# Optimization experiments

Measured on AMD Instinct MI355X. Metric: run time of the kernel, lower is better.

The kernel has to match this reference:

```python
import jax, jax.numpy as jnp
import numpy as np

B, H, S, D = 4, 16, 2048, 64
SCALE = 8.0  # sqrt(D)
NEG = -1000000000.0


def setup_inputs() -> dict:
    key = jax.random.key(0)
    kq, kk, kv = jax.random.split(key, 3)
    q = jax.random.normal(kq, (B, H, S, D), dtype=jnp.float32)
    k = jax.random.normal(kk, (B, H, S, D), dtype=jnp.float32)
    v = jax.random.normal(kv, (B, H, S, D), dtype=jnp.float32)
    # causal mask: True means masked out (matches torch masked_fill)
    mask = jnp.triu(jnp.ones((S, S), dtype=bool), k=1)[None, None, :, :]
    mask = jnp.broadcast_to(mask, (B, 1, S, S))
    return {"q": q, "k": k, "v": v, "mask": mask}


def reference(q, k, v, mask):
    # score = q @ k^T / scale  -> [B,H,S,S]
    score = jnp.einsum("bhqd,bhkd->bhqk", q, k) / SCALE
    score = jnp.where(mask, NEG, score)
    probs = jax.nn.softmax(score, axis=-1)
    context = jnp.einsum("bhqk,bhkd->bhqd", probs, v)
    return context
```

## Files before the change

### kernel.cpp

```cpp
#include <hip/hip_runtime.h>

#define SQ 2048
#define DH 64
#define BK 64
#define NQT 32
#define NBH 64
#define M0 8.0f

#define WS_BYTES ((size_t)2 * NBH * SQ * DH * 2)

typedef float f32x4 __attribute__((ext_vector_type(4)));
typedef __bf16 bf16x8 __attribute__((ext_vector_type(8)));
typedef _Float16 f16x4 __attribute__((ext_vector_type(4)));
typedef _Float16 f16x8 __attribute__((ext_vector_type(8)));
typedef __fp16 fp16x2 __attribute__((ext_vector_type(2)));
typedef unsigned short u16x8 __attribute__((ext_vector_type(8)));
typedef unsigned int u32x4 __attribute__((ext_vector_type(4)));

static __device__ __forceinline__ unsigned int pkbf(float a, float b) {
#if __has_builtin(__builtin_amdgcn_cvt_pk_bf16_f32)
  typedef __bf16 bf16x2 __attribute__((ext_vector_type(2)));
  bf16x2 r = __builtin_amdgcn_cvt_pk_bf16_f32(a, b);
  return __builtin_bit_cast(unsigned int, r);
#else
  unsigned int ua = __builtin_bit_cast(unsigned int, a);
  unsigned int ub = __builtin_bit_cast(unsigned int, b);
  ua += 0x7fffu + ((ua >> 16) & 1u);
  ub += 0x7fffu + ((ub >> 16) & 1u);
  return (ua >> 16) | (ub & 0xffff0000u);
#endif
}

static __device__ __forceinline__ unsigned int pkf16(float a, float b) {
  fp16x2 r = __builtin_amdgcn_cvt_pkrtz(a, b);
  return __builtin_bit_cast(unsigned int, r);
}

static __device__ __forceinline__ f32x4 mfma_qk(u16x8 a, u16x8 b, f32x4 c) {
  return __builtin_amdgcn_mfma_f32_16x16x32_bf16(
      __builtin_bit_cast(bf16x8, a), __builtin_bit_cast(bf16x8, b), c, 0, 0, 0);
}

static __device__ __forceinline__ f32x4 mfma_pv(f16x4 a, f16x4 b, f32x4 c) {
  return __builtin_amdgcn_mfma_f32_16x16x16f16(a, b, c, 0, 0, 0);
}

static __device__ __forceinline__ f32x4 mfma_pv32(f16x8 a, f16x8 b, f32x4 c) {
  return __builtin_amdgcn_mfma_f32_16x16x32_f16(a, b, c, 0, 0, 0);
}

static __device__ __forceinline__ void ld16(unsigned short* l, const unsigned short* g) {
  __builtin_amdgcn_global_load_lds(
      (const __attribute__((address_space(1))) unsigned int*)(const void*)g,
      (__attribute__((address_space(3))) unsigned int*)(void*)l, 16, 0, 0);
}

static __device__ __forceinline__ void store_tile(float* wb, float* dst,
                                                  const f32x4* o, int lane,
                                                  int l15, int quad) {
#pragma unroll
  for (int dt = 0; dt < 4; ++dt) {
    const int colw = dt * 16 + quad * 4;
    *(f32x4*)&wb[l15 * 64 + (colw ^ ((l15 & 3) * 16))] = o[dt];
  }
  __builtin_amdgcn_wave_barrier();
#pragma unroll
  for (int j = 0; j < 4; ++j) {
    const int row = j * 4 + (lane >> 4);
    const int colw = (lane & 15) * 4;
    f32x4 v = *(const f32x4*)&wb[row * 64 + (colw ^ ((row & 3) * 16))];
    *(f32x4*)&dst[row * 64 + colw] = v;
  }
}

__global__ __launch_bounds__(256) void prep(const float* __restrict__ K,
                                            const float* __restrict__ V,
                                            unsigned short* __restrict__ Kf,
                                            unsigned short* __restrict__ Vf) {
  const int bh = (int)blockIdx.x >> 5;
  const int st = (int)blockIdx.x & 31;
  const int tid = threadIdx.x;
  __shared__ __align__(16) unsigned short T[DH * 64];
  {
    const int kvb = (tid >> 4) * 4, vdb = (tid & 15) * 4;
    const float* vp = V + ((size_t)bh * SQ + st * 64 + kvb) * DH + vdb;
    f32x4 r0 = *(const f32x4*)vp, r1 = *(const f32x4*)(vp + DH),
          r2 = *(const f32x4*)(vp + 2 * DH), r3 = *(const f32x4*)(vp + 3 * DH);
    const int uu = kvb >> 3, h = (kvb >> 2) & 1;
#pragma unroll
    for (int i = 0; i < 4; ++i) {
      const int d = vdb + i;
      uint2 w = {pkf16(r0[i], r1[i]), pkf16(r2[i], r3[i])};
      *(uint2*)&T[d * 64 + ((uu ^ (d & 7)) * 8) + h * 4] = w;
    }
  }
  {
    const size_t kin = ((size_t)bh * SQ + st * 64) * DH;
    unsigned short* kfo = Kf + (size_t)bh * SQ * DH + (size_t)st * 64 * DH;
#pragma unroll
    for (int e = 0; e < 2; ++e) {
      const int L = tid * 2 + e;
      const int l15 = L & 15, quad = (L >> 4) & 3, c = (L >> 6) & 1, nt = (L >> 7) & 3;
      const int krow = (nt >> 1) * 32 + ((l15 >> 2) & 3) * 8 + (nt & 1) * 4 + (l15 & 3);
      const float* kp = K + kin + (size_t)krow * DH + (c * 4 + quad) * 8;
      f32x4 x = *(const f32x4*)kp, y = *(const f32x4*)(kp + 4);
      u32x4 w = {pkbf(x[0], x[1]), pkbf(x[2], x[3]), pkbf(y[0], y[1]), pkbf(y[2], y[3])};
      *(u32x4*)&kfo[L * 8] = w;
    }
  }
  __syncthreads();
  {
    unsigned short* vfo = Vf + (size_t)bh * SQ * DH + (size_t)st * 64 * DH;
#pragma unroll
    for (int e = 0; e < 2; ++e) {
      const int L = tid * 2 + e;
      const int l15 = L & 15, quad = (L >> 4) & 3, dt = (L >> 6) & 3, n2 = (L >> 8) & 1;
      const int d = dt * 16 + l15, uu = n2 * 4 + quad;
      u16x8 val = *(const u16x8*)&T[d * 64 + ((uu ^ (d & 7)) * 8)];
      *(u16x8*)&vfo[L * 8] = val;
    }
  }
}

__global__ __launch_bounds__(256, 4) void fa_main(
    const float* __restrict__ Q, const unsigned short* __restrict__ Kf,
    const unsigned short* __restrict__ Vf, float* __restrict__ O) {
  const int lin = (int)blockIdx.x;
  const int xcd = lin & 7, u = lin >> 3;
  const int hh = u & 7;
  const int pi = (int)((0x32104567BA98CDEFull >> ((u >> 3) * 4)) & 15u);
  const int bh = hh * 8 + xcd;
  const int tend = 2 * pi + 1;

  const int tid = threadIdx.x;
  const int wv = tid >> 6;
  const int lane = tid & 63;
  const int l15 = lane & 15;
  const int quad = lane >> 4;

  __shared__ __align__(16) unsigned short S0[2 * BK * DH];
  __shared__ __align__(16) unsigned short S1[2 * BK * DH];

  const size_t hq = (size_t)bh * (SQ * DH);
  const unsigned short* KfH = Kf + (size_t)bh * SQ * DH;
  const unsigned short* VfH = Vf + (size_t)bh * SQ * DH;

  const int qbase = pi * 128 + wv * 32;
  const int dtw = 2 * pi + (wv >> 1);
  const int qo = (wv & 1) * 32;

  u16x8 qf[2][2];
  {
    const float scq = 0.125f * 1.4426950408889634f;
#pragma unroll
    for (int f = 0; f < 2; ++f) {
      const float* qp = Q + hq + (size_t)(qbase + 16 * f + l15) * DH + quad * 8;
#pragma unroll
      for (int c = 0; c < 2; ++c) {
        f32x4 x = *(const f32x4*)(qp + c * 32);
        f32x4 y = *(const f32x4*)(qp + c * 32 + 4);
        u32x4 w = {pkbf(x[0] * scq, x[1] * scq), pkbf(x[2] * scq, x[3] * scq),
                   pkbf(y[0] * scq, y[1] * scq), pkbf(y[2] * scq, y[3] * scq)};
        qf[f][c] = __builtin_bit_cast(u16x8, w);
      }
    }
  }

  f32x4 o0[4], o1[4], la0, la1;
#pragma unroll
  for (int dt = 0; dt < 4; ++dt) {
    o0[dt] = (f32x4){0.f, 0.f, 0.f, 0.f};
    o1[dt] = (f32x4){0.f, 0.f, 0.f, 0.f};
  }
  la0 = (f32x4){0.f, 0.f, 0.f, 0.f};
  la1 = (f32x4){0.f, 0.f, 0.f, 0.f};
  const f16x8 ones8 = {(_Float16)1.f, (_Float16)1.f, (_Float16)1.f, (_Float16)1.f,
                       (_Float16)1.f, (_Float16)1.f, (_Float16)1.f, (_Float16)1.f};

  auto stage = [&](unsigned short* W, int t) {
#pragma unroll
    for (int j = 0; j < 2; ++j)
      ld16(&W[j * 2048 + tid * 8], &KfH[(size_t)t * 4096 + j * 2048 + tid * 8]);
#pragma unroll
    for (int j = 0; j < 2; ++j)
      ld16(&W[4096 + j * 2048 + tid * 8],
           &VfH[(size_t)t * 4096 + j * 2048 + tid * 8]);
  };

  auto attend = [&](const unsigned short* B, bool diag) {
    const unsigned short* Ks = B;
    const unsigned short* Vs = B + 4096;
    f32x4 s0[4], s1[4];
    __builtin_amdgcn_s_setprio(1);
#pragma unroll
    for (int nt = 0; nt < 4; ++nt) {
      f32x4 a0 = {-M0, -M0, -M0, -M0}, a1 = {-M0, -M0, -M0, -M0};
#pragma unroll
      for (int c = 0; c < 2; ++c) {
        u16x8 kf = *(const u16x8*)&Ks[(nt * 2 + c) * 512 + lane * 8];
        a0 = mfma_qk(kf, qf[0][c], a0);
        a1 = mfma_qk(kf, qf[1][c], a1);
      }
      s0[nt] = a0;
      s1[nt] = a1;
    }
    __builtin_amdgcn_s_setprio(0);
    if (diag) {
#pragma unroll
      for (int nt = 0; nt < 4; ++nt)
#pragma unroll
        for (int r = 0; r < 4; ++r) {
          const int kvl = (nt >> 1) * 32 + quad * 8 + (nt & 1) * 4 + r;
          if (kvl > qo + l15) s0[nt][r] = -1e30f;
          if (kvl > qo + 16 + l15) s1[nt][r] = -1e30f;
        }
    }
    f16x8 pf0[2], pf1[2];
#pragma unroll
    for (int n2 = 0; n2 < 2; ++n2) {
      f32x4 pe0, po0, pe1, po1;
#pragma unroll
      for (int r = 0; r < 4; ++r) {
        pe0[r] = __builtin_amdgcn_exp2f(s0[2 * n2][r]);
        po0[r] = __builtin_amdgcn_exp2f(s0[2 * n2 + 1][r]);
        pe1[r] = __builtin_amdgcn_exp2f(s1[2 * n2][r]);
        po1[r] = __builtin_amdgcn_exp2f(s1[2 * n2 + 1][r]);
      }
      u32x4 w0 = {pkf16(pe0[0], pe0[1]), pkf16(pe0[2], pe0[3]),
                  pkf16(po0[0], po0[1]), pkf16(po0[2], po0[3])};
      u32x4 w1 = {pkf16(pe1[0], pe1[1]), pkf16(pe1[2], pe1[3]),
                  pkf16(po1[0], po1[1]), pkf16(po1[2], po1[3])};
      pf0[n2] = __builtin_bit_cast(f16x8, w0);
      pf1[n2] = __builtin_bit_cast(f16x8, w1);
    }
    __builtin_amdgcn_s_setprio(1);
#pragma unroll
    for (int n2 = 0; n2 < 2; ++n2) {
      la0 = mfma_pv32(ones8, pf0[n2], la0);
      la1 = mfma_pv32(ones8, pf1[n2], la1);
    }
#pragma unroll
    for (int dt = 0; dt < 4; ++dt) {
#pragma unroll
      for (int n2 = 0; n2 < 2; ++n2) {
        f16x8 vf = *(const f16x8*)&Vs[(n2 * 4 + dt) * 512 + lane * 8];
        o0[dt] = mfma_pv32(vf, pf0[n2], o0[dt]);
        o1[dt] = mfma_pv32(vf, pf1[n2], o1[dt]);
      }
    }
    __builtin_amdgcn_s_setprio(0);
  };

  auto step = [&](int t, const unsigned short* R, unsigned short* W) {
    if (t <= dtw) attend(R, t == dtw);
    __syncthreads();
    if (t + 2 <= tend) stage(W, t + 2);
  };

  stage(S0, 0);
  __syncthreads();
  stage(S1, 1);
  for (int t = 0; t <= tend; t += 2) {
    step(t, S0, S0);
    if (t + 1 <= tend) step(t + 1, S1, S1);
  }

  {
    const float inv0 = 1.0f / la0[0];
    const float inv1 = 1.0f / la1[0];
#pragma unroll
    for (int f = 0; f < 2; ++f) {
      const f32x4* oo = f ? o1 : o0;
      const float inv = f ? inv1 : inv0;
      float* dst = O + hq + (size_t)(qbase + f * 16 + l15) * DH + quad * 4;
#pragma unroll
      for (int dt = 0; dt < 4; ++dt) {
        f32x4 v = oo[dt] * inv;
        *(f32x4*)(dst + dt * 16) = v;
      }
    }
  }
}

__global__ __launch_bounds__(256, 4) void fa_full(
    const float* __restrict__ Q, const float* __restrict__ K,
    const float* __restrict__ V, float* __restrict__ O) {
  const int lin = (int)blockIdx.x;
  const int xcd = lin & 7;
  const int u = lin >> 3;
  const int hh = u & 7;
  const int p = u >> 3;
  const int bh = hh * 8 + xcd;
  const int tid = threadIdx.x;
  const int wv = tid >> 6;
  const int lane = tid & 63;
  const int l15 = lane & 15;
  const int quad = lane >> 4;
  __shared__ __align__(16) unsigned short SMEM[2][2 * BK * DH];
  const size_t hbase = (size_t)bh * (SQ * DH);
  const int krr = tid >> 3, kcc = (tid & 7) * 8;
  const int kvb = (tid >> 4) * 4, vdb = (tid & 15) * 4;
#pragma unroll
  for (int ph = 0; ph < 2; ++ph) {
    const int qt = ph ? (NQT - 1 - p) : p;
    const int wq0 = qt * 64 + wv * 16;
    u16x8 qf[2];
    {
      const float scq = 0.125f * 1.4426950408889634f;
      const float* qp = Q + hbase + (size_t)(wq0 + l15) * DH + quad * 8;
#pragma unroll
      for (int c = 0; c < 2; ++c) {
        f32x4 x = *(const f32x4*)(qp + c * 32);
        f32x4 y = *(const f32x4*)(qp + c * 32 + 4);
        u32x4 w = {pkbf(x[0] * scq, x[1] * scq), pkbf(x[2] * scq, x[3] * scq),
                   pkbf(y[0] * scq, y[1] * scq), pkbf(y[2] * scq, y[3] * scq)};
        qf[c] = __builtin_bit_cast(u16x8, w);
      }
    }
    f32x4 o[4];
#pragma unroll
    for (int dt = 0; dt < 4; ++dt) o[dt] = (f32x4){0.f, 0.f, 0.f, 0.f};
    float l = 0.f;
    f32x4 ka[2][2], va[4];
    {
      const float* kp = K + hbase + (size_t)krr * DH + kcc;
      ka[0][0] = *(const f32x4*)kp;             ka[0][1] = *(const f32x4*)(kp + 4);
      ka[1][0] = *(const f32x4*)(kp + 32 * DH); ka[1][1] = *(const f32x4*)(kp + 32 * DH + 4);
      const float* vp = V + hbase + (size_t)kvb * DH + vdb;
      va[0] = *(const f32x4*)vp;            va[1] = *(const f32x4*)(vp + DH);
      va[2] = *(const f32x4*)(vp + 2 * DH); va[3] = *(const f32x4*)(vp + 3 * DH);
    }
    __syncthreads();
    {
      unsigned short* Ksn = SMEM[0];
      unsigned short* Vsn = SMEM[0] + BK * DH;
#pragma unroll
      for (int h = 0; h < 2; ++h) {
        const int rr = h * 32 + krr;
        u32x4 w = {pkbf(ka[h][0][0], ka[h][0][1]), pkbf(ka[h][0][2], ka[h][0][3]),
                   pkbf(ka[h][1][0], ka[h][1][1]), pkbf(ka[h][1][2], ka[h][1][3])};
        *(u32x4*)&Ksn[rr * DH + (kcc ^ ((rr & 7) * 8))] = w;
      }
#pragma unroll
      for (int i = 0; i < 4; ++i) {
        const int d = vdb + i;
        uint2 w = {pkf16(va[0][i], va[1][i]), pkf16(va[2][i], va[3][i])};
        *(uint2*)&Vsn[d * BK + (kvb ^ ((d & 15) * 4))] = w;
      }
    }
    __syncthreads();
    for (int t = 0; t <= qt; ++t) {
      const unsigned short* Ks = SMEM[t & 1];
      const unsigned short* Vs = SMEM[t & 1] + BK * DH;
      if (t < qt) {
        const int kb2 = (t + 1) * BK;
        const float* kp = K + hbase + (size_t)(kb2 + krr) * DH + kcc;
        ka[0][0] = *(const f32x4*)kp;             ka[0][1] = *(const f32x4*)(kp + 4);
        ka[1][0] = *(const f32x4*)(kp + 32 * DH); ka[1][1] = *(const f32x4*)(kp + 32 * DH + 4);
        const float* vp = V + hbase + (size_t)(kb2 + kvb) * DH + vdb;
        va[0] = *(const f32x4*)vp;            va[1] = *(const f32x4*)(vp + DH);
        va[2] = *(const f32x4*)(vp + 2 * DH); va[3] = *(const f32x4*)(vp + 3 * DH);
      }
      f32x4 s[4];
#pragma unroll
      for (int nt = 0; nt < 4; ++nt) {
        f32x4 acc = {-M0, -M0, -M0, -M0};
#pragma unroll
        for (int c = 0; c < 2; ++c) {
          const int row = nt * 16 + l15;
          u16x8 kf = *(const u16x8*)&Ks[row * DH + ((c * 32 + quad * 8) ^ ((l15 & 7) * 8))];
          acc = mfma_qk(kf, qf[c], acc);
        }
        s[nt] = acc;
      }
      if (t == qt) {
#pragma unroll
        for (int nt = 0; nt < 4; ++nt)
#pragma unroll
          for (int r = 0; r < 4; ++r)
            if (nt * 16 + quad * 4 + r > wv * 16 + l15) s[nt][r] = -1e30f;
      }
      f16x4 pf[4];
#pragma unroll
      for (int nt = 0; nt < 4; ++nt) {
        f32x4 pr;
#pragma unroll
        for (int r = 0; r < 4; ++r) { pr[r] = __builtin_amdgcn_exp2f(s[nt][r]); l += pr[r]; }
        uint2 w2 = {pkf16(pr[0], pr[1]), pkf16(pr[2], pr[3])};
        pf[nt] = __builtin_bit_cast(f16x4, w2);
      }
#pragma unroll
      for (int dt = 0; dt < 4; ++dt) {
        const int d = dt * 16 + l15;
#pragma unroll
        for (int nt = 0; nt < 4; ++nt) {
          f16x4 vf = *(const f16x4*)&Vs[d * BK + ((nt * 16 + quad * 4) ^ (l15 * 4))];
          o[dt] = mfma_pv(vf, pf[nt], o[dt]);
        }
      }
      if (t < qt) {
        unsigned short* Ksn = SMEM[(t + 1) & 1];
        unsigned short* Vsn = SMEM[(t + 1) & 1] + BK * DH;
#pragma unroll
        for (int h = 0; h < 2; ++h) {
          const int rr = h * 32 + krr;
          u32x4 w = {pkbf(ka[h][0][0], ka[h][0][1]), pkbf(ka[h][0][2], ka[h][0][3]),
                     pkbf(ka[h][1][0], ka[h][1][1]), pkbf(ka[h][1][2], ka[h][1][3])};
          *(u32x4*)&Ksn[rr * DH + (kcc ^ ((rr & 7) * 8))] = w;
        }
#pragma unroll
        for (int i = 0; i < 4; ++i) {
          const int d = vdb + i;
          uint2 w = {pkf16(va[0][i], va[1][i]), pkf16(va[2][i], va[3][i])};
          *(uint2*)&Vsn[d * BK + (kvb ^ ((d & 15) * 4))] = w;
        }
        __syncthreads();
      }
    }
    l += __shfl_xor(l, 16, 64);
    l += __shfl_xor(l, 32, 64);
    const float inv = 1.0f / l;
    f32x4 on[4];
#pragma unroll
    for (int dt = 0; dt < 4; ++dt) on[dt] = o[dt] * inv;
    float* wb = (float*)SMEM[(qt + 1) & 1] + wv * 1024;
    store_tile(wb, O + hbase + (size_t)wq0 * DH, on, lane, l15, quad);
  }
}

extern "C" void kernel_launch(void* const* d_in, const int* in_sizes, int n_in,
                              void* d_out, int out_size, void* d_ws, size_t ws_size,
                              hipStream_t stream) {
  const float* q = (const float*)d_in[0];
  const float* k = (const float*)d_in[1];
  const float* v = (const float*)d_in[2];
  float* o = (float*)d_out;
  if (ws_size >= WS_BYTES) {
    unsigned short* Kf = (unsigned short*)d_ws;
    unsigned short* Vf = Kf + (size_t)NBH * SQ * DH;
    prep<<<dim3(NBH * 32), 256, 0, stream>>>(k, v, Kf, Vf);
    fa_main<<<dim3(1024), 256, 0, stream>>>(q, Kf, Vf, o);
  } else {
    fa_full<<<dim3(1024), 256, 0, stream>>>(q, k, v, o);
  }
}
```

Before: 201.2 us.

## Split long causal query tiles across two blocks with atomic partial accumulation

Query tiles 4..15 are now each split into two KV-range halves handled by separate blocks, which atomically add unnormalized outputs and row sums into a zeroed output and a workspace buffer. A separate norm kernel then divides those rows by the accumulated sums. The aim is to balance the causal triangular workload and fill more CUs with 1792 blocks instead of 1024. In exchange it adds two memsets, float atomics on the output, and an extra pass over the output. The fixed max M0 means partial results can be summed without rescaling.

```diff
diff --git a/kernel.cpp b/kernel.cpp
--- a/kernel.cpp
+++ b/kernel.cpp
@@ -8,6 +8,7 @@
 #define M0 8.0f
 
 #define WS_BYTES ((size_t)2 * NBH * SQ * DH * 2)
+#define WS_BYTES2 (WS_BYTES + (size_t)NBH * SQ * 4)
 
 typedef float f32x4 __attribute__((ext_vector_type(4)));
 typedef __bf16 bf16x8 __attribute__((ext_vector_type(8)));
@@ -16,6 +17,11 @@
 typedef __fp16 fp16x2 __attribute__((ext_vector_type(2)));
 typedef unsigned short u16x8 __attribute__((ext_vector_type(8)));
 typedef unsigned int u32x4 __attribute__((ext_vector_type(4)));
+
+__device__ const unsigned char JT[28] = {
+    0x1F, 0x2F, 0x1E, 0x2E, 0x1D, 0x2D, 0x1C, 0x2C, 0x1B, 0x2B,
+    0x1A, 0x2A, 0x19, 0x29, 0x18, 0x28, 0x17, 0x27, 0x03, 0x16,
+    0x26, 0x02, 0x15, 0x25, 0x14, 0x24, 0x01, 0x00};
 
 static __device__ __forceinline__ unsigned int pkbf(float a, float b) {
 #if __has_builtin(__builtin_amdgcn_cvt_pk_bf16_f32)
@@ -124,13 +130,17 @@
 
 __global__ __launch_bounds__(256, 4) void fa_main(
     const float* __restrict__ Q, const unsigned short* __restrict__ Kf,
-    const unsigned short* __restrict__ Vf, float* __restrict__ O) {
+    const unsigned short* __restrict__ Vf, float* __restrict__ O,
+    float* __restrict__ Lb) {
   const int lin = (int)blockIdx.x;
-  const int xcd = lin & 7, u = lin >> 3;
-  const int hh = u & 7;
-  const int pi = (int)((0x32104567BA98CDEFull >> ((u >> 3) * 4)) & 15u);
+  const int xcd = lin & 7, hh = (lin >> 3) & 7, jid = lin >> 6;
   const int bh = hh * 8 + xcd;
-  const int tend = 2 * pi + 1;
+  const int jv = JT[jid];
+  const int pi = jv & 15;
+  const int kind = jv >> 4;
+  const int t0 = (kind == 2) ? pi + 1 : 0;
+  const int t1 = (kind == 1) ? pi : 2 * pi + 1;
+  const bool partial = (kind != 0);
 
   const int tid = threadIdx.x;
   const int wv = tid >> 6;
@@ -138,6 +148,9 @@
   const int l15 = lane & 15;
   const int quad = lane >> 4;
 
+  const int dtwv = (kind == 1) ? t1 : (2 * pi + (wv >> 1));
+  const bool hasd = (kind != 1);
+
   __shared__ __align__(16) unsigned short S0[2 * BK * DH];
   __shared__ __align__(16) unsigned short S1[2 * BK * DH];
 
@@ -146,7 +159,6 @@
   const unsigned short* VfH = Vf + (size_t)bh * SQ * DH;
 
   const int qbase = pi * 128 + wv * 32;
-  const int dtw = 2 * pi + (wv >> 1);
   const int qo = (wv & 1) * 32;
 
   u16x8 qf[2][2];
@@ -252,20 +264,20 @@
   };
 
   auto step = [&](int t, const unsigned short* R, unsigned short* W) {
-    if (t <= dtw) attend(R, t == dtw);
+    if (t <= dtwv) attend(R, hasd && t == dtwv);
     __syncthreads();
-    if (t + 2 <= tend) stage(W, t + 2);
+    if (t + 2 <= t1) stage(W, t + 2);
   };
 
-  stage(S0, 0);
+  stage(S0, t0);
   __syncthreads();
-  stage(S1, 1);
-  for (int t = 0; t <= tend; t += 2) {
+  stage(S1, t0 + 1);
+  for (int t = t0; t <= t1; t += 2) {
     step(t, S0, S0);
-    if (t + 1 <= tend) step(t + 1, S1, S1);
-  }
-
-  {
+    if (t + 1 <= t1) step(t + 1, S1, S1);
+  }
+
+  if (!partial) {
     const float inv0 = 1.0f / la0[0];
     const float inv1 = 1.0f / la1[0];
 #pragma unroll
@@ -279,7 +291,35 @@
         *(f32x4*)(dst + dt * 16) = v;
       }
     }
-  }
+  } else {
+#pragma unroll
+    for (int f = 0; f < 2; ++f) {
+      const f32x4* oo = f ? o1 : o0;
+      float* dst = O + hq + (size_t)(qbase + f * 16 + l15) * DH + quad * 4;
+#pragma unroll
+      for (int dt = 0; dt < 4; ++dt)
+#pragma unroll
+        for (int i = 0; i < 4; ++i)
+          unsafeAtomicAdd(dst + dt * 16 + i, oo[dt][i]);
+    }
+    if (quad == 0) {
+      unsafeAtomicAdd(&Lb[bh * SQ + qbase + l15], la0[0]);
+      unsafeAtomicAdd(&Lb[bh * SQ + qbase + 16 + l15], la1[0]);
+    }
+  }
+}
+
+__global__ __launch_bounds__(256) void norm(float* __restrict__ O,
+                                            const float* __restrict__ Lb) {
+  const int bid = (int)blockIdx.x;
+  const int bh = bid / 48, sub = bid % 48;
+  const int e = sub * 2048 + (int)threadIdx.x * 8;
+  const int row = 512 + (e >> 6);
+  const float inv = 1.0f / Lb[bh * SQ + row];
+  float* p = O + (size_t)bh * (SQ * DH) + (size_t)512 * DH + e;
+  f32x4 a = *(f32x4*)p, b = *(f32x4*)(p + 4);
+  *(f32x4*)p = a * inv;
+  *(f32x4*)(p + 4) = b * inv;
 }
 
 __global__ __launch_bounds__(256, 4) void fa_full(
@@ -435,11 +475,15 @@
   const float* k = (const float*)d_in[1];
   const float* v = (const float*)d_in[2];
   float* o = (float*)d_out;
-  if (ws_size >= WS_BYTES) {
+  if (ws_size >= WS_BYTES2) {
     unsigned short* Kf = (unsigned short*)d_ws;
     unsigned short* Vf = Kf + (size_t)NBH * SQ * DH;
+    float* Lb = (float*)(Vf + (size_t)NBH * SQ * DH);
+    hipMemsetAsync(d_out, 0, (size_t)out_size, stream);
+    hipMemsetAsync(Lb, 0, (size_t)NBH * SQ * 4, stream);
     prep<<<dim3(NBH * 32), 256, 0, stream>>>(k, v, Kf, Vf);
-    fa_main<<<dim3(1024), 256, 0, stream>>>(q, Kf, Vf, o);
+    fa_main<<<dim3(28 * NBH), 256, 0, stream>>>(q, Kf, Vf, o, Lb);
+    norm<<<dim3(NBH * 48), 256, 0, stream>>>(o, Lb);
   } else {
     fa_full<<<dim3(1024), 256, 0, stream>>>(q, k, v, o);
   }
```

After: 352.3 us. 1.75x slower.
